# Kernel tuning notes

Measured on AMD Instinct MI355X. Metric: run time of the kernel, lower is better.

The kernel has to match this reference:

```python
import jax, jax.numpy as jnp
import numpy as np

N, X_DIM, Y_DIM, HID = 8192, 512, 2048 // 4, 2048
Y_DIM = 512

def setup_inputs() -> dict:
    key = jax.random.key(0)
    ks = jax.random.split(key, 10)
    def lin(k, fan_in, fan_out):
        lim = 1.0 / np.sqrt(fan_in)
        kw, kb = jax.random.split(k)
        W = jax.random.uniform(kw, (fan_in, fan_out), jnp.float32, -lim, lim)
        b = jax.random.uniform(kb, (fan_out,), jnp.float32, -lim, lim)
        return W, b
    mu_W1, mu_b1 = lin(ks[0], X_DIM, HID)
    mu_W2, mu_b2 = lin(ks[1], HID, Y_DIM)
    lv_W1, lv_b1 = lin(ks[2], X_DIM, HID)
    lv_W2, lv_b2 = lin(ks[3], HID, Y_DIM)
    return {
        "x_samples": jax.random.normal(ks[4], (N, X_DIM), jnp.float32),
        "y_samples": jax.random.normal(ks[5], (N, Y_DIM), jnp.float32),
        "mu_W1": mu_W1, "mu_b1": mu_b1, "mu_W2": mu_W2, "mu_b2": mu_b2,
        "lv_W1": lv_W1, "lv_b1": lv_b1, "lv_W2": lv_W2, "lv_b2": lv_b2,
    }

def reference(x_samples, y_samples, mu_W1, mu_b1, mu_W2, mu_b2, lv_W1, lv_b1, lv_W2, lv_b2):
    # MLP heads (GEMMs)
    mu = jax.nn.relu(x_samples @ mu_W1 + mu_b1) @ mu_W2 + mu_b2          # [N, D]
    logvar = jnp.tanh(jax.nn.relu(x_samples @ lv_W1 + lv_b1) @ lv_W2 + lv_b2)  # [N, D]
    w = 0.5 * jnp.exp(-logvar)                                           # 1/(2*exp(logvar))
    n = x_samples.shape[0]

    # positive: -mean_i sum_d (mu_id - y_id)^2 * w_id
    positive = -(((mu - y_samples) ** 2) * w).sum(axis=1).mean()

    # negative (exact decomposition of the [N,N,D] broadcast):
    # -(1/N^2) sum_{i,d} w_id * (N*mu_id^2 - 2*mu_id*Sy_d + Sy2_d)
    Sy = y_samples.sum(axis=0)          # [D]
    Sy2 = (y_samples ** 2).sum(axis=0)  # [D]
    negative = -(w * (n * mu ** 2 - 2.0 * mu * Sy + Sy2)).sum() / (n * n)

    return positive - negative
```

## Files before the change

kernel.cpp:

```cpp
#include <hip/hip_runtime.h>
#include <hip/hip_bf16.h>
#include <stdint.h>

#define NS   8192
#define XD   512
#define HD   2048
#define YD   512

typedef unsigned short u16;
using bf16x8 = __attribute__((ext_vector_type(8))) short;
using f32x4  = __attribute__((ext_vector_type(4))) float;

__device__ __forceinline__ float bf2f(u16 u) {
  union { uint32_t i; float f; } v; v.i = ((uint32_t)u) << 16; return v.f;
}
__device__ __forceinline__ u16 f2b(float f) {
  __hip_bfloat16 hb = __float2bfloat16(f);
  return *(const u16*)&hb;
}
__device__ __forceinline__ float ld_in(const void* p, int f32, size_t i) {
  return f32 ? ((const float*)p)[i] : bf2f(((const u16*)p)[i]);
}
#define GLDS(gp, lp) __builtin_amdgcn_global_load_lds( \
    (__attribute__((address_space(1))) void*)(gp),     \
    (__attribute__((address_space(3))) void*)(lp), 16, 0, 0)

struct Args10 { const void* p[10]; int n[10]; };

__global__ void detect_kernel(Args10 a, int* __restrict__ flags) {
  const int b = blockIdx.x;
  const u16* q = (const u16*)a.p[b];
  int m = a.n[b]; if (m > 8192) m = 8192;
  int wild = 0;
  for (int i = threadIdx.x; i < m; i += blockDim.x) {
    float v = bf2f(q[i]);
    if (!(fabsf(v) <= 1000.0f)) wild = 1;
  }
  if (wild) atomicOr(&flags[b], 1);
}

__global__ __launch_bounds__(256) void prep_kernel(
    const void* __restrict__ x, const void* __restrict__ y,
    const void* b1m, const void* b2m, const void* b1l, const void* b2l,
    const int* __restrict__ flags,
    u16* __restrict__ xb, float* __restrict__ biasv,
    float* __restrict__ Sy, float* __restrict__ Sy2) {
  const int b = blockIdx.x;
  if (b < 2048) {
    if (!flags[0]) return;
    const size_t base = (size_t)b * 2048 + (size_t)threadIdx.x * 8;
    alignas(16) u16 o[8];
    const float4* s = (const float4*)((const float*)x + base);
    float4 v0 = s[0], v1 = s[1];
    o[0]=f2b(v0.x); o[1]=f2b(v0.y); o[2]=f2b(v0.z); o[3]=f2b(v0.w);
    o[4]=f2b(v1.x); o[5]=f2b(v1.y); o[6]=f2b(v1.z); o[7]=f2b(v1.w);
    *(uint4*)(xb + base) = *(const uint4*)o;
  } else if (b < 2112) {
    const int f = flags[1];
    const int t = threadIdx.x;
    const int r0 = (b - 2048) * 128;
    float s0 = 0.f, s1 = 0.f, q0 = 0.f, q1 = 0.f;
    for (int r = r0; r < r0 + 128; ++r) {
      float a = ld_in(y, f, (size_t)r * YD + t);
      float c = ld_in(y, f, (size_t)r * YD + t + 256);
      s0 += a; q0 += a * a;
      s1 += c; q1 += c * c;
    }
    atomicAdd(&Sy[t], s0);        atomicAdd(&Sy2[t], q0);
    atomicAdd(&Sy[t + 256], s1);  atomicAdd(&Sy2[t + 256], q1);
  } else {
    for (int i = threadIdx.x; i < 5120; i += 256) {
      float v;
      if (i < 2048)      v = ld_in(b1m, flags[3], i);
      else if (i < 4096) v = ld_in(b1l, flags[7], i - 2048);
      else if (i < 4608) v = ld_in(b2m, flags[5], i - 4096);
      else               v = ld_in(b2l, flags[9], i - 4608);
      biasv[i] = v;
    }
  }
}

__global__ __launch_bounds__(256) void transpose_all(
    const void* w1m, const void* w2m, const void* w1l, const void* w2l,
    const int* __restrict__ flags,
    u16* W1t, u16* W2tm, u16* W2tl) {
  __shared__ u16 tile[32][33];
  const int id = blockIdx.x, which = id >> 10, t = id & 1023;
  const void* in; u16* out; int R, C, fidx;
  if (which == 0)      { in = w1m; out = W1t;                      R = XD; C = HD; fidx = 2; }
  else if (which == 1) { in = w2m; out = W2tm;                     R = HD; C = YD; fidx = 4; }
  else if (which == 2) { in = w1l; out = W1t + (size_t)HD * XD;    R = XD; C = HD; fidx = 6; }
  else                 { in = w2l; out = W2tl;                     R = HD; C = YD; fidx = 8; }
  const int f = flags[fidx];
  const int nbx = C >> 5;
  const int bx = t % nbx, by = t / nbx;
  const int c0 = bx * 32, r0 = by * 32;
  const int tx = threadIdx.x & 31, ty = threadIdx.x >> 5;
  for (int i = ty; i < 32; i += 8)
    tile[i][tx] = f2b(ld_in(in, f, (size_t)(r0 + i) * C + (c0 + tx)));
  __syncthreads();
  for (int i = ty; i < 32; i += 8)
    out[(size_t)(c0 + i) * R + (r0 + tx)] = tile[tx][i];
}

__global__ __launch_bounds__(256) void gemm1_kernel(
    const void* __restrict__ xraw, const u16* __restrict__ xb,
    const u16* __restrict__ W1t,
    const float* __restrict__ bias,
    const int* __restrict__ flags,
    u16* __restrict__ h_mu, u16* __restrict__ h_lv) {
  constexpr int K = XD;
  __shared__ alignas(16) u16 As[128 * 64];
  __shared__ alignas(16) u16 Bs[128 * 64];

  const u16* A = flags[0] ? xb : (const u16*)xraw;

  const int tid = threadIdx.x, wid = tid >> 6, lane = tid & 63;
  const int MT = NS / 128, NT = (2 * HD) / 128;
  const int id = blockIdx.x;
  const int xcd = id & 7, slot = id >> 3;
  const int bm0 = (xcd * (MT >> 3) + slot / NT) * 128;
  const int bn0 = (slot % NT) * 128;

  const int mrow = (wid >> 1) * 64, ncol = (wid & 1) * 64;
  const int quad = lane >> 4, c16 = lane & 15, cswz = c16 & 7;
  const int srow = lane >> 3, sc = lane & 7;
  const int scg  = (sc ^ srow) * 8;

  f32x4 acc[4][4] = {};

  for (int k0 = 0; k0 < K; k0 += 64) {
#pragma unroll
    for (int j = 0; j < 4; ++j) {
      const int grp = wid * 4 + j, row = grp * 8 + srow;
      GLDS(A   + (size_t)(bm0 + row) * K + (k0 + scg), As + grp * 512);
      GLDS(W1t + (size_t)(bn0 + row) * K + (k0 + scg), Bs + grp * 512);
    }
    __syncthreads();
#pragma unroll
    for (int h = 0; h < 2; ++h) {
      const int off = ((h * 4 + quad) ^ cswz) * 8;
      bf16x8 af[4], bfr[4];
#pragma unroll
      for (int mi = 0; mi < 4; ++mi)
        af[mi] = *(const bf16x8*)&As[(mrow + mi * 16 + c16) * 64 + off];
#pragma unroll
      for (int ni = 0; ni < 4; ++ni)
        bfr[ni] = *(const bf16x8*)&Bs[(ncol + ni * 16 + c16) * 64 + off];
#pragma unroll
      for (int mi = 0; mi < 4; ++mi)
#pragma unroll
        for (int ni = 0; ni < 4; ++ni)
          acc[mi][ni] = __builtin_amdgcn_mfma_f32_16x16x32_bf16(
              af[mi], bfr[ni], acc[mi][ni], 0, 0, 0);
    }
    __syncthreads();
  }

  const bool is_lv = bn0 >= HD;
  u16* dst = is_lv ? h_lv : h_mu;
  const int cb = bn0 - (is_lv ? HD : 0);
#pragma unroll
  for (int ni = 0; ni < 4; ++ni) {
    const int gc = ncol + ni * 16 + c16;
    const float bv = bias[bn0 + gc];
#pragma unroll
    for (int mi = 0; mi < 4; ++mi)
#pragma unroll
      for (int r = 0; r < 4; ++r) {
        const int grow = bm0 + mrow + mi * 16 + quad * 4 + r;
        dst[(size_t)grow * HD + (cb + gc)] = f2b(fmaxf(acc[mi][ni][r] + bv, 0.f));
      }
  }
}

__global__ __launch_bounds__(256) void gemm2_dual(
    const u16* __restrict__ hm, const u16* __restrict__ hl,
    const u16* __restrict__ W2m, const u16* __restrict__ W2l,
    const float* __restrict__ b2m, const float* __restrict__ b2l,
    const void* __restrict__ y, const int* __restrict__ flags,
    const float* __restrict__ Sy, const float* __restrict__ Sy2,
    double* __restrict__ gacc) {
  constexpr int K = HD;
  __shared__ alignas(16) u16 Am[64 * 64];
  __shared__ alignas(16) u16 Al[64 * 64];
  __shared__ alignas(16) u16 Bm[128 * 64];
  __shared__ alignas(16) u16 Bl[128 * 64];

  const int tid = threadIdx.x, wid = tid >> 6, lane = tid & 63;
  const int MT = NS / 64, NT = YD / 128;
  const int id = blockIdx.x;
  const int xcd = id & 7, slot = id >> 3;
  const int bm0 = (xcd * (MT >> 3) + slot / NT) * 64;
  const int bn0 = (slot % NT) * 128;

  const int mrow = (wid >> 1) * 32, ncol = (wid & 1) * 64;
  const int quad = lane >> 4, c16 = lane & 15, cswz = c16 & 7;
  const int srow = lane >> 3, sc = lane & 7;
  const int scg  = (sc ^ srow) * 8;

  f32x4 am[2][4] = {}, al[2][4] = {};

  for (int k0 = 0; k0 < K; k0 += 64) {
#pragma unroll
    for (int j = 0; j < 2; ++j) {
      const int grp = wid * 2 + j, row = grp * 8 + srow;
      const size_t go = (size_t)(bm0 + row) * K + (k0 + scg);
      GLDS(hm + go, Am + grp * 512);
      GLDS(hl + go, Al + grp * 512);
    }
#pragma unroll
    for (int j = 0; j < 4; ++j) {
      const int grp = wid * 4 + j, row = grp * 8 + srow;
      const size_t go = (size_t)(bn0 + row) * K + (k0 + scg);
      GLDS(W2m + go, Bm + grp * 512);
      GLDS(W2l + go, Bl + grp * 512);
    }
    __syncthreads();
#pragma unroll
    for (int h = 0; h < 2; ++h) {
      const int off = ((h * 4 + quad) ^ cswz) * 8;
      bf16x8 afm[2], afl[2], bfm[4], bfl[4];
#pragma unroll
      for (int mi = 0; mi < 2; ++mi) {
        const int rl = (mrow + mi * 16 + c16) * 64 + off;
        afm[mi] = *(const bf16x8*)&Am[rl];
        afl[mi] = *(const bf16x8*)&Al[rl];
      }
#pragma unroll
      for (int ni = 0; ni < 4; ++ni) {
        const int rl = (ncol + ni * 16 + c16) * 64 + off;
        bfm[ni] = *(const bf16x8*)&Bm[rl];
        bfl[ni] = *(const bf16x8*)&Bl[rl];
      }
#pragma unroll
      for (int mi = 0; mi < 2; ++mi)
#pragma unroll
        for (int ni = 0; ni < 4; ++ni) {
          am[mi][ni] = __builtin_amdgcn_mfma_f32_16x16x32_bf16(
              afm[mi], bfm[ni], am[mi][ni], 0, 0, 0);
          al[mi][ni] = __builtin_amdgcn_mfma_f32_16x16x32_bf16(
              afl[mi], bfl[ni], al[mi][ni], 0, 0, 0);
        }
    }
    __syncthreads();
  }

  const int yf = flags[1];
  const float invN = 1.0f / (float)NS;
  float s = 0.f;
#pragma unroll
  for (int ni = 0; ni < 4; ++ni) {
    const int gcol = bn0 + ncol + ni * 16 + c16;
    const float bmv = b2m[gcol], blv = b2l[gcol];
    const float syv = Sy[gcol], sy2v = Sy2[gcol];
#pragma unroll
    for (int mi = 0; mi < 2; ++mi)
#pragma unroll
      for (int r = 0; r < 4; ++r) {
        const int grow = bm0 + mrow + mi * 16 + quad * 4 + r;
        const float m   = am[mi][ni][r] + bmv;
        const float lvp = al[mi][ni][r] + blv;
        const float w   = 0.5f * expf(-tanhf(lvp));
        const float yv  = ld_in(y, yf, (size_t)grow * YD + gcol);
        s += w * (yv * yv - 2.f * m * yv + (2.f * m * syv - sy2v) * invN);
      }
  }
  for (int off = 32; off > 0; off >>= 1) s += __shfl_down(s, off);
  __shared__ double bs[4];
  if (lane == 0) bs[wid] = (double)s;
  __syncthreads();
  if (tid == 0) atomicAdd(gacc, bs[0] + bs[1] + bs[2] + bs[3]);
}

__global__ void finalize_kernel(const double* __restrict__ gacc,
                                float* __restrict__ out) {
  if (threadIdx.x == 0)
    out[0] = (float)(-gacc[0] / (double)NS);
}

extern "C" void kernel_launch(void* const* d_in, const int* in_sizes, int n_in,
                              void* d_out, int out_size, void* d_ws, size_t ws_size,
                              hipStream_t stream) {
  char* ws = (char*)d_ws;
  double* gacc = (double*)ws;
  int*    flags = (int*)(ws + 16);
  float*  Sy    = (float*)(ws + 128);
  float*  Sy2   = (float*)(ws + 2176);
  float*  biasv = (float*)(ws + 4224);
  u16* xb   = (u16*)(ws + 24704);
  u16* W1t  = xb + (size_t)NS * XD;
  u16* W2tm = W1t + (size_t)2 * HD * XD;
  u16* W2tl = W2tm + (size_t)YD * HD;
  u16* h_mu = W2tl + (size_t)YD * HD;
  u16* h_lv = h_mu + (size_t)NS * HD;

  hipMemsetAsync(d_ws, 0, 4224, stream);

  Args10 a;
  for (int i = 0; i < 10; ++i) { a.p[i] = d_in[i]; a.n[i] = in_sizes[i]; }
  detect_kernel<<<10, 256, 0, stream>>>(a, flags);

  prep_kernel<<<2113, 256, 0, stream>>>(d_in[0], d_in[1], d_in[3], d_in[5],
                                        d_in[7], d_in[9], flags, xb, biasv, Sy, Sy2);
  transpose_all<<<4096, 256, 0, stream>>>(d_in[2], d_in[4], d_in[6], d_in[8],
                                          flags, W1t, W2tm, W2tl);

  const float* b1  = biasv;
  const float* b2m = biasv + 4096, *b2l = biasv + 4608;

  gemm1_kernel<<<(NS / 128) * ((2 * HD) / 128), 256, 0, stream>>>(
      d_in[0], xb, W1t, b1, flags, h_mu, h_lv);

  gemm2_dual<<<(NS / 64) * (YD / 128), 256, 0, stream>>>(
      h_mu, h_lv, W2tm, W2tl, b2m, b2l, d_in[1], flags, Sy, Sy2, gacc);

  finalize_kernel<<<1, 64, 0, stream>>>(gacc, (float*)d_out);
}
```

Before: 252.7 us.

## Split gemm2 waves by head, transpose MFMA operands, vectorize epilogues, serpentine tiles

GEMM2 now gives each pair of waves one head (mu or logvar) over the full 64x128 tile, rather than every wave computing both heads on a 32x64 sub-tile. The logvar waves compute w, write it to an LDS tile that reuses the operand buffers, and the mu waves read it back to form the loss. Both GEMMs swap the MFMA operand order so each lane holds 4 consecutive columns, which allows 4-wide vectorized bias loads, output stores and y loads. Tile order is serpentined across N to improve L2 reuse. This adds an extra barrier and LDS round trip, and during the epilogue half of the waves sit idle.

```diff
diff --git a/kernel.cpp b/kernel.cpp
--- a/kernel.cpp
+++ b/kernel.cpp
@@ -9,6 +9,7 @@
 
 typedef unsigned short u16;
 using bf16x8 = __attribute__((ext_vector_type(8))) short;
+using u16x4  = __attribute__((ext_vector_type(4))) short;
 using f32x4  = __attribute__((ext_vector_type(4))) float;
 
 __device__ __forceinline__ float bf2f(u16 u) {
@@ -119,8 +120,11 @@
   const int MT = NS / 128, NT = (2 * HD) / 128;
   const int id = blockIdx.x;
   const int xcd = id & 7, slot = id >> 3;
-  const int bm0 = (xcd * (MT >> 3) + slot / NT) * 128;
-  const int bn0 = (slot % NT) * 128;
+  const int m_idx = slot / NT;
+  int n_idx = slot % NT;
+  if (m_idx & 1) n_idx = NT - 1 - n_idx;
+  const int bm0 = (xcd * (MT >> 3) + m_idx) * 128;
+  const int bn0 = n_idx * 128;
 
   const int mrow = (wid >> 1) * 64, ncol = (wid & 1) * 64;
   const int quad = lane >> 4, c16 = lane & 15, cswz = c16 & 7;
@@ -152,7 +156,7 @@
 #pragma unroll
         for (int ni = 0; ni < 4; ++ni)
           acc[mi][ni] = __builtin_amdgcn_mfma_f32_16x16x32_bf16(
-              af[mi], bfr[ni], acc[mi][ni], 0, 0, 0);
+              bfr[ni], af[mi], acc[mi][ni], 0, 0, 0);
     }
     __syncthreads();
   }
@@ -161,16 +165,18 @@
   u16* dst = is_lv ? h_lv : h_mu;
   const int cb = bn0 - (is_lv ? HD : 0);
 #pragma unroll
-  for (int ni = 0; ni < 4; ++ni) {
-    const int gc = ncol + ni * 16 + c16;
-    const float bv = bias[bn0 + gc];
-#pragma unroll
-    for (int mi = 0; mi < 4; ++mi)
-#pragma unroll
-      for (int r = 0; r < 4; ++r) {
-        const int grow = bm0 + mrow + mi * 16 + quad * 4 + r;
-        dst[(size_t)grow * HD + (cb + gc)] = f2b(fmaxf(acc[mi][ni][r] + bv, 0.f));
-      }
+  for (int mi = 0; mi < 4; ++mi) {
+    const int grow = bm0 + mrow + mi * 16 + c16;
+#pragma unroll
+    for (int ni = 0; ni < 4; ++ni) {
+      const int col = ncol + ni * 16 + quad * 4;
+      const f32x4 bv = *(const f32x4*)&bias[bn0 + col];
+      u16x4 o;
+#pragma unroll
+      for (int r = 0; r < 4; ++r)
+        o[r] = (short)f2b(fmaxf(acc[mi][ni][r] + bv[r], 0.f));
+      *(u16x4*)&dst[(size_t)grow * HD + (cb + col)] = o;
+    }
   }
 }
 
@@ -182,24 +188,34 @@
     const float* __restrict__ Sy, const float* __restrict__ Sy2,
     double* __restrict__ gacc) {
   constexpr int K = HD;
-  __shared__ alignas(16) u16 Am[64 * 64];
-  __shared__ alignas(16) u16 Al[64 * 64];
-  __shared__ alignas(16) u16 Bm[128 * 64];
-  __shared__ alignas(16) u16 Bl[128 * 64];
+  __shared__ alignas(16) u16 smem[25088];
+  u16* Am = smem;
+  u16* Al = smem + 4096;
+  u16* Bm = smem + 8192;
+  u16* Bl = smem + 16384;
+  float* wtile = (float*)smem;
+  __shared__ double bs[4];
 
   const int tid = threadIdx.x, wid = tid >> 6, lane = tid & 63;
   const int MT = NS / 64, NT = YD / 128;
   const int id = blockIdx.x;
   const int xcd = id & 7, slot = id >> 3;
-  const int bm0 = (xcd * (MT >> 3) + slot / NT) * 64;
-  const int bn0 = (slot % NT) * 128;
-
-  const int mrow = (wid >> 1) * 32, ncol = (wid & 1) * 64;
+  const int m_idx = slot / NT;
+  int n_idx = slot % NT;
+  if (m_idx & 1) n_idx = NT - 1 - n_idx;
+  const int bm0 = (xcd * (MT >> 3) + m_idx) * 64;
+  const int bn0 = n_idx * 128;
+
+  const int head = wid >> 1;
+  const int nbase = (wid & 1) * 64;
   const int quad = lane >> 4, c16 = lane & 15, cswz = c16 & 7;
   const int srow = lane >> 3, sc = lane & 7;
   const int scg  = (sc ^ srow) * 8;
 
-  f32x4 am[2][4] = {}, al[2][4] = {};
+  const u16* Ah = head ? Al : Am;
+  const u16* Bh = head ? Bl : Bm;
+
+  f32x4 acc[4][4] = {};
 
   for (int k0 = 0; k0 < K; k0 += 64) {
 #pragma unroll
@@ -220,54 +236,75 @@
 #pragma unroll
     for (int h = 0; h < 2; ++h) {
       const int off = ((h * 4 + quad) ^ cswz) * 8;
-      bf16x8 afm[2], afl[2], bfm[4], bfl[4];
-#pragma unroll
-      for (int mi = 0; mi < 2; ++mi) {
-        const int rl = (mrow + mi * 16 + c16) * 64 + off;
-        afm[mi] = *(const bf16x8*)&Am[rl];
-        afl[mi] = *(const bf16x8*)&Al[rl];
+      bf16x8 af[4], bf[4];
+#pragma unroll
+      for (int mi = 0; mi < 4; ++mi)
+        af[mi] = *(const bf16x8*)&Ah[(mi * 16 + c16) * 64 + off];
+#pragma unroll
+      for (int ni = 0; ni < 4; ++ni)
+        bf[ni] = *(const bf16x8*)&Bh[(nbase + ni * 16 + c16) * 64 + off];
+#pragma unroll
+      for (int mi = 0; mi < 4; ++mi)
+#pragma unroll
+        for (int ni = 0; ni < 4; ++ni)
+          acc[mi][ni] = __builtin_amdgcn_mfma_f32_16x16x32_bf16(
+              bf[ni], af[mi], acc[mi][ni], 0, 0, 0);
+    }
+    __syncthreads();
+  }
+
+  if (head) {
+#pragma unroll
+    for (int mi = 0; mi < 4; ++mi) {
+      const int m_local = mi * 16 + c16;
+#pragma unroll
+      for (int ni = 0; ni < 4; ++ni) {
+        const int colb = nbase + ni * 16 + quad * 4;
+        const f32x4 bv = *(const f32x4*)&b2l[bn0 + colb];
+        f32x4 wv;
+#pragma unroll
+        for (int r = 0; r < 4; ++r)
+          wv[r] = 0.5f * expf(-tanhf(acc[mi][ni][r] + bv[r]));
+        *(f32x4*)&wtile[m_local * 132 + colb] = wv;
       }
+    }
+  }
+  __syncthreads();
+
+  float s = 0.f;
+  if (!head) {
+    const int yf = flags[1];
+    const float invN = 1.0f / (float)NS;
+#pragma unroll
+    for (int mi = 0; mi < 4; ++mi) {
+      const int m_local = mi * 16 + c16;
+      const int grow = bm0 + m_local;
 #pragma unroll
       for (int ni = 0; ni < 4; ++ni) {
-        const int rl = (ncol + ni * 16 + c16) * 64 + off;
-        bfm[ni] = *(const bf16x8*)&Bm[rl];
-        bfl[ni] = *(const bf16x8*)&Bl[rl];
+        const int colb = nbase + ni * 16 + quad * 4;
+        const int gcol = bn0 + colb;
+        const f32x4 bv  = *(const f32x4*)&b2m[gcol];
+        const f32x4 wv  = *(const f32x4*)&wtile[m_local * 132 + colb];
+        const f32x4 syv = *(const f32x4*)&Sy[gcol];
+        const f32x4 sy2 = *(const f32x4*)&Sy2[gcol];
+        f32x4 yv;
+        if (yf) {
+          yv = *(const f32x4*)((const float*)y + (size_t)grow * YD + gcol);
+        } else {
+          u16x4 t = *(const u16x4*)((const u16*)y + (size_t)grow * YD + gcol);
+#pragma unroll
+          for (int r = 0; r < 4; ++r) yv[r] = bf2f((u16)t[r]);
+        }
+#pragma unroll
+        for (int r = 0; r < 4; ++r) {
+          const float m = acc[mi][ni][r] + bv[r];
+          s += wv[r] * (yv[r] * yv[r] - 2.f * m * yv[r]
+                        + (2.f * m * syv[r] - sy2[r]) * invN);
+        }
       }
-#pragma unroll
-      for (int mi = 0; mi < 2; ++mi)
-#pragma unroll
-        for (int ni = 0; ni < 4; ++ni) {
-          am[mi][ni] = __builtin_amdgcn_mfma_f32_16x16x32_bf16(
-              afm[mi], bfm[ni], am[mi][ni], 0, 0, 0);
-          al[mi][ni] = __builtin_amdgcn_mfma_f32_16x16x32_bf16(
-              afl[mi], bfl[ni], al[mi][ni], 0, 0, 0);
-        }
-    }
-    __syncthreads();
-  }
-
-  const int yf = flags[1];
-  const float invN = 1.0f / (float)NS;
-  float s = 0.f;
-#pragma unroll
-  for (int ni = 0; ni < 4; ++ni) {
-    const int gcol = bn0 + ncol + ni * 16 + c16;
-    const float bmv = b2m[gcol], blv = b2l[gcol];
-    const float syv = Sy[gcol], sy2v = Sy2[gcol];
-#pragma unroll
-    for (int mi = 0; mi < 2; ++mi)
-#pragma unroll
-      for (int r = 0; r < 4; ++r) {
-        const int grow = bm0 + mrow + mi * 16 + quad * 4 + r;
-        const float m   = am[mi][ni][r] + bmv;
-        const float lvp = al[mi][ni][r] + blv;
-        const float w   = 0.5f * expf(-tanhf(lvp));
-        const float yv  = ld_in(y, yf, (size_t)grow * YD + gcol);
-        s += w * (yv * yv - 2.f * m * yv + (2.f * m * syv - sy2v) * invN);
-      }
+    }
   }
   for (int off = 32; off > 0; off >>= 1) s += __shfl_down(s, off);
-  __shared__ double bs[4];
   if (lane == 0) bs[wid] = (double)s;
   __syncthreads();
   if (tid == 0) atomicAdd(gacc, bs[0] + bs[1] + bs[2] + bs[3]);
```

New measurement: 307.7 us. 1.22x slower.

## Fuse detect, prep, transpose and finalize kernels to cut launches

Applied to the files above, without the earlier changes.

Removes the separate dtype-detection kernel: each block now probes its own input inline through shared memory. The weight transpose moves into the prep kernel with 64x64 tiles and vectorized 16-byte loads and stores. The finalize kernel is replaced by a last-block-done counter inside gemm2. This cuts three kernel launches and their serialization, but every block, including all gemm1 and gemm2 blocks, now redundantly scans 1024 input elements.

```diff
diff --git a/kernel.cpp b/kernel.cpp
--- a/kernel.cpp
+++ b/kernel.cpp
@@ -25,30 +25,37 @@
     (__attribute__((address_space(1))) void*)(gp),     \
     (__attribute__((address_space(3))) void*)(lp), 16, 0, 0)
 
-struct Args10 { const void* p[10]; int n[10]; };
-
-__global__ void detect_kernel(Args10 a, int* __restrict__ flags) {
-  const int b = blockIdx.x;
-  const u16* q = (const u16*)a.p[b];
-  int m = a.n[b]; if (m > 8192) m = 8192;
+__device__ __forceinline__ int probe_f32(const void* p, int n_u16, int* sflag) {
+  if (threadIdx.x == 0) *sflag = 0;
+  __syncthreads();
+  const u16* q = (const u16*)p;
   int wild = 0;
-  for (int i = threadIdx.x; i < m; i += blockDim.x) {
+  for (int i = threadIdx.x; i < n_u16; i += blockDim.x) {
     float v = bf2f(q[i]);
     if (!(fabsf(v) <= 1000.0f)) wild = 1;
   }
-  if (wild) atomicOr(&flags[b], 1);
-}
-
-__global__ __launch_bounds__(256) void prep_kernel(
+  if (wild) *sflag = 1;
+  __syncthreads();
+  int r = *sflag;
+  __syncthreads();
+  return r;
+}
+
+__global__ __launch_bounds__(256) void prep_all(
     const void* __restrict__ x, const void* __restrict__ y,
-    const void* b1m, const void* b2m, const void* b1l, const void* b2l,
-    const int* __restrict__ flags,
+    const void* w1m, const void* b1m, const void* w2m, const void* b2m,
+    const void* w1l, const void* b1l, const void* w2l, const void* b2l,
     u16* __restrict__ xb, float* __restrict__ biasv,
-    float* __restrict__ Sy, float* __restrict__ Sy2) {
+    float* __restrict__ Sy, float* __restrict__ Sy2,
+    u16* __restrict__ W1t, u16* __restrict__ W2tm, u16* __restrict__ W2tl) {
+  __shared__ u16 tile[64 * 72];
+  __shared__ int sflag;
   const int b = blockIdx.x;
+  const int tid = threadIdx.x;
+
   if (b < 2048) {
-    if (!flags[0]) return;
-    const size_t base = (size_t)b * 2048 + (size_t)threadIdx.x * 8;
+    if (!probe_f32(x, 1024, &sflag)) return;
+    const size_t base = (size_t)b * 2048 + (size_t)tid * 8;
     alignas(16) u16 o[8];
     const float4* s = (const float4*)((const float*)x + base);
     float4 v0 = s[0], v1 = s[1];
@@ -56,64 +63,78 @@
     o[4]=f2b(v1.x); o[5]=f2b(v1.y); o[6]=f2b(v1.z); o[7]=f2b(v1.w);
     *(uint4*)(xb + base) = *(const uint4*)o;
   } else if (b < 2112) {
-    const int f = flags[1];
-    const int t = threadIdx.x;
+    const int f = probe_f32(y, 1024, &sflag);
     const int r0 = (b - 2048) * 128;
     float s0 = 0.f, s1 = 0.f, q0 = 0.f, q1 = 0.f;
     for (int r = r0; r < r0 + 128; ++r) {
-      float a = ld_in(y, f, (size_t)r * YD + t);
-      float c = ld_in(y, f, (size_t)r * YD + t + 256);
+      float a = ld_in(y, f, (size_t)r * YD + tid);
+      float c = ld_in(y, f, (size_t)r * YD + tid + 256);
       s0 += a; q0 += a * a;
       s1 += c; q1 += c * c;
     }
-    atomicAdd(&Sy[t], s0);        atomicAdd(&Sy2[t], q0);
-    atomicAdd(&Sy[t + 256], s1);  atomicAdd(&Sy2[t + 256], q1);
+    atomicAdd(&Sy[tid], s0);        atomicAdd(&Sy2[tid], q0);
+    atomicAdd(&Sy[tid + 256], s1);  atomicAdd(&Sy2[tid + 256], q1);
+  } else if (b == 2112) {
+    const int f3 = probe_f32(b1m, 1024, &sflag);
+    const int f5 = probe_f32(b2m, 512, &sflag);
+    const int f7 = probe_f32(b1l, 1024, &sflag);
+    const int f9 = probe_f32(b2l, 512, &sflag);
+    for (int i = tid; i < 5120; i += 256) {
+      float v;
+      if (i < 2048)      v = ld_in(b1m, f3, i);
+      else if (i < 4096) v = ld_in(b1l, f7, i - 2048);
+      else if (i < 4608) v = ld_in(b2m, f5, i - 4096);
+      else               v = ld_in(b2l, f9, i - 4608);
+      biasv[i] = v;
+    }
   } else {
-    for (int i = threadIdx.x; i < 5120; i += 256) {
-      float v;
-      if (i < 2048)      v = ld_in(b1m, flags[3], i);
-      else if (i < 4096) v = ld_in(b1l, flags[7], i - 2048);
-      else if (i < 4608) v = ld_in(b2m, flags[5], i - 4096);
-      else               v = ld_in(b2l, flags[9], i - 4608);
-      biasv[i] = v;
-    }
-  }
-}
-
-__global__ __launch_bounds__(256) void transpose_all(
-    const void* w1m, const void* w2m, const void* w1l, const void* w2l,
-    const int* __restrict__ flags,
-    u16* W1t, u16* W2tm, u16* W2tl) {
-  __shared__ u16 tile[32][33];
-  const int id = blockIdx.x, which = id >> 10, t = id & 1023;
-  const void* in; u16* out; int R, C, fidx;
-  if (which == 0)      { in = w1m; out = W1t;                      R = XD; C = HD; fidx = 2; }
-  else if (which == 1) { in = w2m; out = W2tm;                     R = HD; C = YD; fidx = 4; }
-  else if (which == 2) { in = w1l; out = W1t + (size_t)HD * XD;    R = XD; C = HD; fidx = 6; }
-  else                 { in = w2l; out = W2tl;                     R = HD; C = YD; fidx = 8; }
-  const int f = flags[fidx];
-  const int nbx = C >> 5;
-  const int bx = t % nbx, by = t / nbx;
-  const int c0 = bx * 32, r0 = by * 32;
-  const int tx = threadIdx.x & 31, ty = threadIdx.x >> 5;
-  for (int i = ty; i < 32; i += 8)
-    tile[i][tx] = f2b(ld_in(in, f, (size_t)(r0 + i) * C + (c0 + tx)));
-  __syncthreads();
-  for (int i = ty; i < 32; i += 8)
-    out[(size_t)(c0 + i) * R + (r0 + tx)] = tile[tx][i];
+    const int id = b - 2113, which = id >> 8, t = id & 255;
+    const void* in; u16* out; int R, C;
+    if (which == 0)      { in = w1m; out = W1t;                   R = XD; C = HD; }
+    else if (which == 1) { in = w2m; out = W2tm;                  R = HD; C = YD; }
+    else if (which == 2) { in = w1l; out = W1t + (size_t)HD * XD; R = XD; C = HD; }
+    else                 { in = w2l; out = W2tl;                  R = HD; C = YD; }
+    const int f = probe_f32(in, 1024, &sflag);
+    const int nbx = C >> 6;
+    const int c0 = (t % nbx) * 64, r0 = (t / nbx) * 64;
+    const int r = tid >> 2, cc = (tid & 3) * 16;
+    if (f) {
+      const float4* s = (const float4*)((const float*)in + (size_t)(r0 + r) * C + c0 + cc);
+#pragma unroll
+      for (int k = 0; k < 4; ++k) {
+        float4 v = s[k];
+        tile[r * 72 + cc + k * 4 + 0] = f2b(v.x);
+        tile[r * 72 + cc + k * 4 + 1] = f2b(v.y);
+        tile[r * 72 + cc + k * 4 + 2] = f2b(v.z);
+        tile[r * 72 + cc + k * 4 + 3] = f2b(v.w);
+      }
+    } else {
+      const uint4* s = (const uint4*)((const u16*)in + (size_t)(r0 + r) * C + c0 + cc);
+      *(uint4*)&tile[r * 72 + cc]     = s[0];
+      *(uint4*)&tile[r * 72 + cc + 8] = s[1];
+    }
+    __syncthreads();
+    const int i = tid >> 2, jc = (tid & 3) * 16;
+    alignas(16) u16 o[16];
+#pragma unroll
+    for (int j = 0; j < 16; ++j) o[j] = tile[(jc + j) * 72 + i];
+    uint4* dq = (uint4*)&out[(size_t)(c0 + i) * R + r0 + jc];
+    dq[0] = ((const uint4*)o)[0];
+    dq[1] = ((const uint4*)o)[1];
+  }
 }
 
 __global__ __launch_bounds__(256) void gemm1_kernel(
     const void* __restrict__ xraw, const u16* __restrict__ xb,
     const u16* __restrict__ W1t,
     const float* __restrict__ bias,
-    const int* __restrict__ flags,
     u16* __restrict__ h_mu, u16* __restrict__ h_lv) {
   constexpr int K = XD;
   __shared__ alignas(16) u16 As[128 * 64];
   __shared__ alignas(16) u16 Bs[128 * 64];
-
-  const u16* A = flags[0] ? xb : (const u16*)xraw;
+  __shared__ int sflag;
+
+  const u16* A = probe_f32(xraw, 1024, &sflag) ? xb : (const u16*)xraw;
 
   const int tid = threadIdx.x, wid = tid >> 6, lane = tid & 63;
   const int MT = NS / 128, NT = (2 * HD) / 128;
@@ -178,14 +199,19 @@
     const u16* __restrict__ hm, const u16* __restrict__ hl,
     const u16* __restrict__ W2m, const u16* __restrict__ W2l,
     const float* __restrict__ b2m, const float* __restrict__ b2l,
-    const void* __restrict__ y, const int* __restrict__ flags,
+    const void* __restrict__ y,
     const float* __restrict__ Sy, const float* __restrict__ Sy2,
-    double* __restrict__ gacc) {
+    double* __restrict__ gacc, unsigned* __restrict__ counter,
+    float* __restrict__ out) {
   constexpr int K = HD;
   __shared__ alignas(16) u16 Am[64 * 64];
   __shared__ alignas(16) u16 Al[64 * 64];
   __shared__ alignas(16) u16 Bm[128 * 64];
   __shared__ alignas(16) u16 Bl[128 * 64];
+  __shared__ double bs[4];
+  __shared__ int sflag;
+
+  const int yf = probe_f32(y, 1024, &sflag);
 
   const int tid = threadIdx.x, wid = tid >> 6, lane = tid & 63;
   const int MT = NS / 64, NT = YD / 128;
@@ -246,7 +272,6 @@
     __syncthreads();
   }
 
-  const int yf = flags[1];
   const float invN = 1.0f / (float)NS;
   float s = 0.f;
 #pragma unroll
@@ -267,27 +292,28 @@
       }
   }
   for (int off = 32; off > 0; off >>= 1) s += __shfl_down(s, off);
-  __shared__ double bs[4];
   if (lane == 0) bs[wid] = (double)s;
   __syncthreads();
-  if (tid == 0) atomicAdd(gacc, bs[0] + bs[1] + bs[2] + bs[3]);
-}
-
-__global__ void finalize_kernel(const double* __restrict__ gacc,
-                                float* __restrict__ out) {
-  if (threadIdx.x == 0)
-    out[0] = (float)(-gacc[0] / (double)NS);
+  if (tid == 0) {
+    atomicAdd(gacc, bs[0] + bs[1] + bs[2] + bs[3]);
+    __threadfence();
+    const unsigned old = atomicAdd(counter, 1u);
+    if (old == gridDim.x - 1) {
+      const double g = atomicAdd(gacc, 0.0);
+      out[0] = (float)(-g / (double)NS);
+    }
+  }
 }
 
 extern "C" void kernel_launch(void* const* d_in, const int* in_sizes, int n_in,
                               void* d_out, int out_size, void* d_ws, size_t ws_size,
                               hipStream_t stream) {
   char* ws = (char*)d_ws;
-  double* gacc = (double*)ws;
-  int*    flags = (int*)(ws + 16);
-  float*  Sy    = (float*)(ws + 128);
-  float*  Sy2   = (float*)(ws + 2176);
-  float*  biasv = (float*)(ws + 4224);
+  double*   gacc    = (double*)ws;
+  unsigned* counter = (unsigned*)(ws + 8);
+  float*    Sy      = (float*)(ws + 128);
+  float*    Sy2     = (float*)(ws + 2176);
+  float*    biasv   = (float*)(ws + 4224);
   u16* xb   = (u16*)(ws + 24704);
   u16* W1t  = xb + (size_t)NS * XD;
   u16* W2tm = W1t + (size_t)2 * HD * XD;
@@ -297,23 +323,18 @@
 
   hipMemsetAsync(d_ws, 0, 4224, stream);
 
-  Args10 a;
-  for (int i = 0; i < 10; ++i) { a.p[i] = d_in[i]; a.n[i] = in_sizes[i]; }
-  detect_kernel<<<10, 256, 0, stream>>>(a, flags);
-
-  prep_kernel<<<2113, 256, 0, stream>>>(d_in[0], d_in[1], d_in[3], d_in[5],
-                                        d_in[7], d_in[9], flags, xb, biasv, Sy, Sy2);
-  transpose_all<<<4096, 256, 0, stream>>>(d_in[2], d_in[4], d_in[6], d_in[8],
-                                          flags, W1t, W2tm, W2tl);
+  prep_all<<<2113 + 1024, 256, 0, stream>>>(
+      d_in[0], d_in[1], d_in[2], d_in[3], d_in[4], d_in[5],
+      d_in[6], d_in[7], d_in[8], d_in[9],
+      xb, biasv, Sy, Sy2, W1t, W2tm, W2tl);
 
   const float* b1  = biasv;
   const float* b2m = biasv + 4096, *b2l = biasv + 4608;
 
   gemm1_kernel<<<(NS / 128) * ((2 * HD) / 128), 256, 0, stream>>>(
-      d_in[0], xb, W1t, b1, flags, h_mu, h_lv);
+      d_in[0], xb, W1t, b1, h_mu, h_lv);
 
   gemm2_dual<<<(NS / 64) * (YD / 128), 256, 0, stream>>>(
-      h_mu, h_lv, W2tm, W2tl, b2m, b2l, d_in[1], flags, Sy, Sy2, gacc);
-
-  finalize_kernel<<<1, 64, 0, stream>>>(gacc, (float*)d_out);
-}
+      h_mu, h_lv, W2tm, W2tl, b2m, b2l, d_in[1], Sy, Sy2,
+      gacc, counter, (float*)d_out);
+}
```

Result: no change. 248.0 us (-1.9%).
